# Optimization experiments

Measured on AMD Instinct MI355X. Metric: run time of the kernel, lower is better.

## Reference

```python
import jax, jax.numpy as jnp
import numpy as np

PREFIX = 20000
LEAF = 50000
NONLEAF = 50000
NUMD = 8 * NONLEAF  # 400000 fine-depth nodes
C = 256


def setup_inputs() -> dict:
    key = jax.random.key(0)
    k1, k2 = jax.random.split(key)
    n_rows = PREFIX + LEAF + NUMD
    x = jax.random.normal(k1, (n_rows, C), dtype=jnp.float32)
    # xavier-uniform-like init for Downsample weights (C_out, C_in, 8)
    limit = float(np.sqrt(6.0 / (C + C * 8)))
    weights = jax.random.uniform(k2, (C, C, 8), dtype=jnp.float32,
                                 minval=-limit, maxval=limit)
    # children at depth-1: alternate leaf (-1) / non-leaf (+1) -> exactly LEAF leaves
    children = jnp.where(jnp.arange(LEAF + NONLEAF) % 2 == 0, -1, 1).astype(jnp.int32)
    return {"x": x, "weights": weights, "children": children,
            "numd": NUMD, "leaf_num": LEAF}


def reference(x, weights, children, numd, leaf_num):
    c = x.shape[1]
    # Downsample: groups of 8 fine nodes -> one coarse node.
    # torch: x.view(-1, 8*C) @ weights.flatten(1).t()
    outd = x[-numd:].reshape(-1, 8 * c) @ weights.reshape(c, 8 * c).T  # [numd/8, C]

    leaf_mask = children < 0                      # [nnum_prev]
    lm = leaf_mask.astype(jnp.int32)
    rank_leaf = jnp.cumsum(lm) - lm               # rank among leaf positions
    nlm = 1 - lm
    rank_nonleaf = jnp.cumsum(nlm) - nlm          # rank among non-leaf positions
    # out[leaf_mask] = x[-leaf_num-numd:-numd]; out[~leaf_mask] = outd
    idx = jnp.where(leaf_mask, rank_leaf, leaf_num + rank_nonleaf)
    x_leaf = x[-(leaf_num + numd):-numd]          # [leaf_num, C]
    combined = jnp.concatenate([x_leaf, outd], axis=0)
    merged = combined[idx]                        # [nnum_prev, C]

    prefix = x.shape[0] - leaf_num - numd
    return jnp.concatenate([x[:prefix], merged], axis=0)
```

## Files before the change

kernel.cpp:

```cpp
#include <hip/hip_runtime.h>
#include <hip/hip_bf16.h>

#define PREFIX_N 20000
#define LEAF_N   50000
#define NONLEAF_N 50000
#define CH_N     (LEAF_N + NONLEAF_N)
#define CCOL     256
#define GK       2048
#define GM       NONLEAF_N
#define OUT_ROWS (PREFIX_N + CH_N)
#define BM       64
#define BKT      64
#define NKT      (GK / BKT)
#define TILES    ((GM + BM - 1) / BM)
#define COPYROWS (PREFIX_N + LEAF_N)
#define COPYBLK  ((COPYROWS + 3) / 4)

typedef float  f32x4v __attribute__((ext_vector_type(4)));
typedef __bf16 bf16x8 __attribute__((ext_vector_type(8)));
typedef short  s16x8  __attribute__((ext_vector_type(8)));

static __device__ __forceinline__ unsigned pk2(float a, float b) {
  __hip_bfloat16 ha = __float2bfloat16(a);
  __hip_bfloat16 hb = __float2bfloat16(b);
  unsigned short sa = __builtin_bit_cast(unsigned short, ha);
  unsigned short sb = __builtin_bit_cast(unsigned short, hb);
  return (unsigned)sa | ((unsigned)sb << 16);
}
static __device__ __forceinline__ uint4 pack8(const float4& x, const float4& y) {
  uint4 r;
  r.x = pk2(x.x, x.y); r.y = pk2(x.z, x.w);
  r.z = pk2(y.x, y.y); r.w = pk2(y.z, y.w);
  return r;
}

__global__ __launch_bounds__(256) void prep_kernel(const float* __restrict__ W,
                                                   unsigned short* __restrict__ Wb,
                                                   const int* __restrict__ ch,
                                                   int* __restrict__ cnt) {
  if (blockIdx.x < 256) {
    int i = blockIdx.x * 256 + threadIdx.x;
    float4 a = ((const float4*)W)[i * 2];
    float4 b = ((const float4*)W)[i * 2 + 1];
    *(uint4*)&Wb[i * 8] = pack8(a, b);
  } else {
    int blk = blockIdx.x - 256;
    int gi = blk * 256 + threadIdx.x;
    int lm = (gi < CH_N && ch[gi] < 0) ? 1 : 0;
    unsigned long long mask = __ballot(lm);
    __shared__ int wsum[4];
    int lane = threadIdx.x & 63, w = threadIdx.x >> 6;
    if (lane == 0) wsum[w] = __popcll(mask);
    __syncthreads();
    if (threadIdx.x == 0) cnt[blk] = wsum[0] + wsum[1] + wsum[2] + wsum[3];
  }
}

__global__ __launch_bounds__(512) void scan_blocks(const int* __restrict__ cnt,
                                                   int* __restrict__ boff, int nb) {
  __shared__ int s[512];
  int t = threadIdx.x;
  int v = (t < nb) ? cnt[t] : 0;
  s[t] = v;
  __syncthreads();
  for (int d = 1; d < 512; d <<= 1) {
    int add = (t >= d) ? s[t - d] : 0;
    __syncthreads();
    s[t] += add;
    __syncthreads();
  }
  if (t < nb) boff[t] = s[t] - v;
}

__global__ __launch_bounds__(256) void rank_kernel(const int* __restrict__ ch,
                                                   const int* __restrict__ boff, int n,
                                                   int* __restrict__ rowof,
                                                   int* __restrict__ leafof) {
  int gi = blockIdx.x * 256 + threadIdx.x;
  int lane = threadIdx.x & 63, w = threadIdx.x >> 6;
  int lm = (gi < n && ch[gi] < 0) ? 1 : 0;
  unsigned long long mask = __ballot(lm);
  int lrank = __popcll(mask & ((1ull << lane) - 1ull));
  __shared__ int wcnt[4];
  if (lane == 63) wcnt[w] = lrank + lm;
  __syncthreads();
  int woff = 0;
  for (int i = 0; i < w; ++i) woff += wcnt[i];
  if (gi < n) {
    int rl = boff[blockIdx.x] + woff + lrank;
    if (lm) leafof[rl] = gi;
    else    rowof[gi - rl] = gi;
  }
}

__global__ __launch_bounds__(256, 3) void main_kernel(const float* __restrict__ x,
                                                      const float* __restrict__ A,
                                                      const unsigned short* __restrict__ Wb,
                                                      const int* __restrict__ rowof,
                                                      const int* __restrict__ leafof,
                                                      float* __restrict__ out) {
  __shared__ unsigned short Al[2][BM * 72];
  __shared__ int tgt[BM];

  const int tid  = threadIdx.x;
  const int lane = tid & 63;

  if (blockIdx.x >= TILES) {
    int j = (blockIdx.x - TILES) * 4 + (tid >> 6);
    if (j >= COPYROWS) return;
    const float* src;
    float* dst;
    if (j < PREFIX_N) {
      src = x + (size_t)j * CCOL;
      dst = out + (size_t)j * CCOL;
    } else {
      int r = j - PREFIX_N;
      src = x + (size_t)(PREFIX_N + r) * CCOL;
      dst = out + (size_t)(PREFIX_N + leafof[r]) * CCOL;
    }
    ((float4*)dst)[lane] = ((const float4*)src)[lane];
    return;
  }

  const int wn = tid >> 6;
  const int lr = lane & 15, lq = lane >> 4;
  const int tile = blockIdx.x;

  if (tid < BM) {
    int m = tile * BM + tid;
    tgt[tid] = (m < GM) ? (PREFIX_N + rowof[m]) : -1;
  }

  const int ar = tid >> 2;
  const int ac = (tid & 3) * 16;
  int agr = tile * BM + ar;
  if (agr >= GM) agr = GM - 1;
  const float* aptr = A + (size_t)agr * GK + ac;
  const int aw = ar * 72 + ac;

  const unsigned short* bbase[4];
#pragma unroll
  for (int fn = 0; fn < 4; ++fn)
    bbase[fn] = Wb + (size_t)(wn * 64 + fn * 16 + lr) * GK + lq * 8;

  int aidx[4];
#pragma unroll
  for (int fm = 0; fm < 4; ++fm)
    aidx[fm] = (fm * 16 + lr) * 72 + lq * 8;

  f32x4v acc[4][4] = {};
  float4 r0, r1, r2, r3;
  r0 = ((const float4*)aptr)[0]; r1 = ((const float4*)aptr)[1];
  r2 = ((const float4*)aptr)[2]; r3 = ((const float4*)aptr)[3];

  int cur = 0;
#pragma unroll 1
  for (int kt = 0; kt < NKT; ++kt) {
    *(uint4*)&Al[cur][aw]     = pack8(r0, r1);
    *(uint4*)&Al[cur][aw + 8] = pack8(r2, r3);
    __syncthreads();

    if (kt + 1 < NKT) {
      const float* p = aptr + (kt + 1) * BKT;
      r0 = ((const float4*)p)[0]; r1 = ((const float4*)p)[1];
      r2 = ((const float4*)p)[2]; r3 = ((const float4*)p)[3];
    }

#pragma unroll
    for (int ks = 0; ks < 2; ++ks) {
      s16x8 af[4], bf[4];
#pragma unroll
      for (int fm = 0; fm < 4; ++fm)
        af[fm] = *(const s16x8*)&Al[cur][aidx[fm] + ks * 32];
#pragma unroll
      for (int fn = 0; fn < 4; ++fn)
        bf[fn] = *(const s16x8*)&bbase[fn][kt * BKT + ks * 32];
#pragma unroll
      for (int fm = 0; fm < 4; ++fm)
#pragma unroll
        for (int fn = 0; fn < 4; ++fn)
          acc[fm][fn] = __builtin_amdgcn_mfma_f32_16x16x32_bf16(
              __builtin_bit_cast(bf16x8, af[fm]),
              __builtin_bit_cast(bf16x8, bf[fn]),
              acc[fm][fn], 0, 0, 0);
    }
    cur ^= 1;
  }

#pragma unroll
  for (int fm = 0; fm < 4; ++fm) {
    int mlb = fm * 16 + lq * 4;
    int t0 = tgt[mlb + 0], t1 = tgt[mlb + 1], t2 = tgt[mlb + 2], t3 = tgt[mlb + 3];
#pragma unroll
    for (int fn = 0; fn < 4; ++fn) {
      int col = wn * 64 + fn * 16 + lr;
      if (t0 >= 0) out[(size_t)t0 * CCOL + col] = acc[fm][fn][0];
      if (t1 >= 0) out[(size_t)t1 * CCOL + col] = acc[fm][fn][1];
      if (t2 >= 0) out[(size_t)t2 * CCOL + col] = acc[fm][fn][2];
      if (t3 >= 0) out[(size_t)t3 * CCOL + col] = acc[fm][fn][3];
    }
  }
}

extern "C" void kernel_launch(void* const* d_in, const int* in_sizes, int n_in,
                              void* d_out, int out_size, void* d_ws, size_t ws_size,
                              hipStream_t stream) {
  const float* x        = (const float*)d_in[0];
  const float* wts      = (const float*)d_in[1];
  const int*   children = (const int*)d_in[2];
  float*       out      = (float*)d_out;

  int* wsp    = (int*)d_ws;
  int* cnt    = wsp;
  int* boff   = wsp + 512;
  int* rowof  = wsp + 1024;
  int* leafof = wsp + 1024 + GM;
  unsigned short* Wb = (unsigned short*)((char*)d_ws + (1 << 20));

  const int nb = (CH_N + 255) / 256;

  prep_kernel<<<256 + nb, 256, 0, stream>>>(wts, Wb, children, cnt);
  scan_blocks<<<1, 512, 0, stream>>>(cnt, boff, nb);
  rank_kernel<<<nb, 256, 0, stream>>>(children, boff, CH_N, rowof, leafof);

  const float* A = x + (size_t)(PREFIX_N + LEAF_N) * CCOL;
  main_kernel<<<TILES + COPYBLK, 256, 0, stream>>>(x, A, Wb, rowof, leafof, out);
}
```

Baseline: 217.0 us.

## Stream fp32 A tiles into swizzled LDS via async global_load_lds, persistent copy blocks

The A operand is now loaded asynchronously straight into LDS as fp32 with global_load_lds, using a larger K tile (256), an XOR swizzle and a two-stage buffer managed with manual vmcnt waits and barriers. Conversion to bf16 moves to after the LDS read, so it no longer goes through registers before the store. The row-copy blocks become a fixed grid of 256 grid-stride blocks instead of one block per four rows. The cost is doubled LDS footprint (fp32, 128KB), which lowers occupancy, plus per-read repacking work and tricky hand-placed waitcnt correctness.

```diff
diff --git a/kernel.cpp b/kernel.cpp
--- a/kernel.cpp
+++ b/kernel.cpp
@@ -3,18 +3,16 @@
 
 #define PREFIX_N 20000
 #define LEAF_N   50000
-#define NONLEAF_N 50000
-#define CH_N     (LEAF_N + NONLEAF_N)
+#define CH_N     100000
 #define CCOL     256
 #define GK       2048
-#define GM       NONLEAF_N
-#define OUT_ROWS (PREFIX_N + CH_N)
+#define GM       50000
 #define BM       64
-#define BKT      64
-#define NKT      (GK / BKT)
+#define BKT      256
+#define NST      (GK / BKT)
 #define TILES    ((GM + BM - 1) / BM)
-#define COPYROWS (PREFIX_N + LEAF_N)
-#define COPYBLK  ((COPYROWS + 3) / 4)
+#define COPYB    256
+#define IT_TOTAL (70000 * 64)
 
 typedef float  f32x4v __attribute__((ext_vector_type(4)));
 typedef __bf16 bf16x8 __attribute__((ext_vector_type(8)));
@@ -33,6 +31,10 @@
   r.z = pk2(y.x, y.y); r.w = pk2(y.z, y.w);
   return r;
 }
+
+#define GLDS16(g, l) __builtin_amdgcn_global_load_lds(                      \
+    (const __attribute__((address_space(1))) void*)(g),                     \
+    (__attribute__((address_space(3))) void*)(l), 16, 0, 0)
 
 __global__ __launch_bounds__(256) void prep_kernel(const float* __restrict__ W,
                                                    unsigned short* __restrict__ Wb,
@@ -93,88 +95,99 @@
   }
 }
 
-__global__ __launch_bounds__(256, 3) void main_kernel(const float* __restrict__ x,
-                                                      const float* __restrict__ A,
-                                                      const unsigned short* __restrict__ Wb,
-                                                      const int* __restrict__ rowof,
-                                                      const int* __restrict__ leafof,
-                                                      float* __restrict__ out) {
-  __shared__ unsigned short Al[2][BM * 72];
+__global__ __launch_bounds__(256) void main_kernel(const float* __restrict__ x,
+                                                   const float* __restrict__ A,
+                                                   const unsigned short* __restrict__ Wb,
+                                                   const int* __restrict__ rowof,
+                                                   const int* __restrict__ leafof,
+                                                   float* __restrict__ out) {
+  __shared__ float Al[2][BM][BKT];
   __shared__ int tgt[BM];
 
   const int tid  = threadIdx.x;
   const int lane = tid & 63;
+  const int w    = tid >> 6;
 
   if (blockIdx.x >= TILES) {
-    int j = (blockIdx.x - TILES) * 4 + (tid >> 6);
-    if (j >= COPYROWS) return;
-    const float* src;
-    float* dst;
-    if (j < PREFIX_N) {
-      src = x + (size_t)j * CCOL;
-      dst = out + (size_t)j * CCOL;
-    } else {
-      int r = j - PREFIX_N;
-      src = x + (size_t)(PREFIX_N + r) * CCOL;
-      dst = out + (size_t)(PREFIX_N + leafof[r]) * CCOL;
+    int cb = blockIdx.x - TILES;
+    const float4* xv = (const float4*)x;
+    float4* ov = (float4*)out;
+    for (int base = cb * 1024; base < IT_TOTAL; base += COPYB * 1024) {
+#pragma unroll
+      for (int u = 0; u < 4; ++u) {
+        int it = base + u * 256 + tid;
+        if (it < IT_TOTAL) {
+          int row = it >> 6, col = it & 63;
+          int drow = (row < PREFIX_N) ? row
+                                      : (PREFIX_N + leafof[row - PREFIX_N]);
+          ov[(size_t)drow * 64 + col] = xv[(size_t)row * 64 + col];
+        }
+      }
     }
-    ((float4*)dst)[lane] = ((const float4*)src)[lane];
     return;
   }
 
-  const int wn = tid >> 6;
-  const int lr = lane & 15, lq = lane >> 4;
   const int tile = blockIdx.x;
+  const int wn   = w;
+  const int lr   = lane & 15, lq = lane >> 4;
 
   if (tid < BM) {
     int m = tile * BM + tid;
     tgt[tid] = (m < GM) ? (PREFIX_N + rowof[m]) : -1;
   }
 
-  const int ar = tid >> 2;
-  const int ac = (tid & 3) * 16;
-  int agr = tile * BM + ar;
-  if (agr >= GM) agr = GM - 1;
-  const float* aptr = A + (size_t)agr * GK + ac;
-  const int aw = ar * 72 + ac;
-
-  const unsigned short* bbase[4];
+  int swz[8];
+#pragma unroll
+  for (int j = 0; j < 8; ++j) swz[j] = (lane ^ j) << 4;
+
+  const char* arow[16];
+#pragma unroll
+  for (int i = 0; i < 16; ++i) {
+    int gr = tile * BM + w * 16 + i;
+    if (gr >= GM) gr = GM - 1;
+    arow[i] = (const char*)(A + (size_t)gr * GK);
+  }
+
+  const unsigned short* bb[4];
 #pragma unroll
   for (int fn = 0; fn < 4; ++fn)
-    bbase[fn] = Wb + (size_t)(wn * 64 + fn * 16 + lr) * GK + lq * 8;
-
-  int aidx[4];
-#pragma unroll
-  for (int fm = 0; fm < 4; ++fm)
-    aidx[fm] = (fm * 16 + lr) * 72 + lq * 8;
+    bb[fn] = Wb + (size_t)(wn * 64 + fn * 16 + lr) * GK + lq * 8;
 
   f32x4v acc[4][4] = {};
-  float4 r0, r1, r2, r3;
-  r0 = ((const float4*)aptr)[0]; r1 = ((const float4*)aptr)[1];
-  r2 = ((const float4*)aptr)[2]; r3 = ((const float4*)aptr)[3];
-
-  int cur = 0;
+
+#define ISSUE_A(kt_, buf_)                                                   \
+  { _Pragma("unroll") for (int i = 0; i < 16; ++i)                           \
+      GLDS16(arow[i] + (size_t)(kt_) * 1024 + swz[i & 7],                    \
+             (char*)&Al[(buf_)][w * 16 + i][0]); }
+
+  ISSUE_A(0, 0);
+  ISSUE_A(1, 1);
+
 #pragma unroll 1
-  for (int kt = 0; kt < NKT; ++kt) {
-    *(uint4*)&Al[cur][aw]     = pack8(r0, r1);
-    *(uint4*)&Al[cur][aw + 8] = pack8(r2, r3);
-    __syncthreads();
-
-    if (kt + 1 < NKT) {
-      const float* p = aptr + (kt + 1) * BKT;
-      r0 = ((const float4*)p)[0]; r1 = ((const float4*)p)[1];
-      r2 = ((const float4*)p)[2]; r3 = ((const float4*)p)[3];
-    }
-
-#pragma unroll
-    for (int ks = 0; ks < 2; ++ks) {
+  for (int kt = 0; kt < NST; ++kt) {
+    if (kt < NST - 1) { asm volatile("s_waitcnt vmcnt(16)" ::: "memory"); }
+    else              { asm volatile("s_waitcnt vmcnt(0)"  ::: "memory"); }
+    __builtin_amdgcn_sched_barrier(0);
+    __builtin_amdgcn_s_barrier();
+    __builtin_amdgcn_sched_barrier(0);
+
+    const float* Ab = &Al[kt & 1][0][0];
+#pragma unroll 2
+    for (int ks = 0; ks < 8; ++ks) {
       s16x8 af[4], bf[4];
 #pragma unroll
-      for (int fm = 0; fm < 4; ++fm)
-        af[fm] = *(const s16x8*)&Al[cur][aidx[fm] + ks * 32];
+      for (int fm = 0; fm < 4; ++fm) {
+        int row = fm * 16 + lr;
+        int c0  = ks * 8 + lq * 2;
+        int p0  = ((c0)     ^ (row & 7)) * 4;
+        int p1  = ((c0 + 1) ^ (row & 7)) * 4;
+        float4 u0 = *(const float4*)&Ab[row * BKT + p0];
+        float4 u1 = *(const float4*)&Ab[row * BKT + p1];
+        af[fm] = __builtin_bit_cast(s16x8, pack8(u0, u1));
+      }
 #pragma unroll
       for (int fn = 0; fn < 4; ++fn)
-        bf[fn] = *(const s16x8*)&bbase[fn][kt * BKT + ks * 32];
+        bf[fn] = *(const s16x8*)&bb[fn][kt * BKT + ks * 32];
 #pragma unroll
       for (int fm = 0; fm < 4; ++fm)
 #pragma unroll
@@ -184,8 +197,13 @@
               __builtin_bit_cast(bf16x8, bf[fn]),
               acc[fm][fn], 0, 0, 0);
     }
-    cur ^= 1;
-  }
+
+    __builtin_amdgcn_sched_barrier(0);
+    __builtin_amdgcn_s_barrier();
+    __builtin_amdgcn_sched_barrier(0);
+    if (kt + 2 < NST) ISSUE_A(kt + 2, kt & 1);
+  }
+#undef ISSUE_A
 
 #pragma unroll
   for (int fm = 0; fm < 4; ++fm) {
@@ -224,5 +242,5 @@
   rank_kernel<<<nb, 256, 0, stream>>>(children, boff, CH_N, rowof, leafof);
 
   const float* A = x + (size_t)(PREFIX_N + LEAF_N) * CCOL;
-  main_kernel<<<TILES + COPYBLK, 256, 0, stream>>>(x, A, Wb, rowof, leafof, out);
-}
+  main_kernel<<<TILES + COPYB, 256, 0, stream>>>(x, A, Wb, rowof, leafof, out);
+}
```

New measurement: 306.1 us. 1.41x slower.
